# Kernel tuning notes

Hardware: AMD Instinct MI355X
Metric: run time of the kernel (lower is better)

## Reference

```python
import jax, jax.numpy as jnp
import numpy as np

B, N, FEAT, HID, K, GH, GW = 4, 4096, 64, 128, 16, 256, 256


def setup_inputs() -> dict:
    key = jax.random.key(0)
    ks = jax.random.split(key, 16)
    # N distinct grid cells per batch -> unique sparse coordinates (scn active sites)
    cells = jax.vmap(lambda k: jax.random.permutation(k, GH * GW)[:N])(jax.random.split(ks[0], B))
    cy = (cells // GW).astype(jnp.float32)
    cx = (cells % GW).astype(jnp.float32)
    x = cx / GW  # round(x*GW) == cx exactly
    y = cy / GH
    z = jnp.zeros((B, N), jnp.float32)
    p = jax.random.uniform(ks[1], (B, N), jnp.float32)
    xyzp = jnp.stack([x, y, z, p], axis=-1).astype(jnp.float32)
    features = jax.random.normal(ks[2], (B, N, FEAT), jnp.float32)

    def w(k, shape, s=0.05):
        return (jax.random.normal(k, shape) * s).astype(jnp.float32)

    return {
        "xyzp": xyzp, "features": features,
        "ln_g": jnp.ones((FEAT + 2,), jnp.float32), "ln_b": jnp.zeros((FEAT + 2,), jnp.float32),
        "W1": w(ks[3], (9, FEAT + 2, HID)), "b1": jnp.zeros((HID,), jnp.float32),
        "W2": w(ks[4], (9, HID, 3 * HID)),
        "pe_w1": w(ks[5], (3, HID)), "pe_b1": jnp.zeros((HID,), jnp.float32),
        "pe_w2": w(ks[6], (HID, HID)), "pe_b2": jnp.zeros((HID,), jnp.float32),
        "at_w1": w(ks[7], (HID, HID)), "at_b1": jnp.zeros((HID,), jnp.float32),
        "at_w2": w(ks[8], (HID, HID)), "at_b2": jnp.zeros((HID,), jnp.float32),
        "ag_w": w(ks[9], (HID, FEAT)), "ag_b": jnp.zeros((FEAT,), jnp.float32),
        "mlp_w1": w(ks[10], (FEAT, HID)), "mlp_b1": jnp.zeros((HID,), jnp.float32),
        "mlp_w2": w(ks[11], (HID, FEAT)), "mlp_b2": jnp.zeros((FEAT,), jnp.float32),
    }


def _knn_gather(xf, idx):
    # xf: [B,N,C], idx: [B,N,K] -> [B,N,K,C]
    return xf[jnp.arange(xf.shape[0])[:, None, None], idx]


def _forward(xyzp, features, ln_g, ln_b, W1, b1, W2, pe_w1, pe_b1, pe_w2, pe_b2,
             at_w1, at_b1, at_w2, at_b2, ag_w, ag_b, mlp_w1, mlp_b1, mlp_w2, mlp_b2):
    # knn in (x,y,0) space -> 2D squared distances, K nearest (self included, sorted)
    xy = xyzp[..., :2]
    s = jnp.sum(xy * xy, axis=-1)
    d2 = s[:, :, None] + s[:, None, :] - 2.0 * jnp.einsum('bnd,bmd->bnm', xy, xy)
    idx = jax.lax.top_k(-d2, K)[1]  # [B,N,K]

    # positional encoding of (x,y,p) relative offsets
    xyp = jnp.stack([xyzp[..., 0], xyzp[..., 1], xyzp[..., 3]], axis=-1)  # [B,N,3]
    rel = xyp[:, :, None, :] - _knn_gather(xyp, idx)  # [B,N,K,3]
    pe = jax.nn.relu(rel @ pe_w1 + pe_b1) @ pe_w2 + pe_b2  # [B,N,K,HID]

    # polarity split + LayerNorm
    p = (xyzp[..., 3:4] - 0.5) / 0.5
    sp = jnp.concatenate([jnp.clip(p, 0.0, 1.0), -jnp.clip(p, -1.0, 0.0), features], axis=-1)
    mu = jnp.mean(sp, axis=-1, keepdims=True)
    var = jnp.var(sp, axis=-1, keepdims=True)
    sp = (sp - mu) / jnp.sqrt(var + 1e-5) * ln_g + ln_b  # [B,N,FEAT+2]

    # submanifold 3x3 conv x2 via dense index grid (active sites only)
    cy = jnp.round(xyzp[..., 1] * GH).astype(jnp.int32)
    cx = jnp.round(xyzp[..., 0] * GW).astype(jnp.int32)
    bb = jnp.broadcast_to(jnp.arange(B)[:, None], (B, N))
    grid = jnp.full((B, GH + 2, GW + 2), -1, jnp.int32)
    grid = grid.at[bb, cy + 1, cx + 1].set(jnp.broadcast_to(jnp.arange(N, dtype=jnp.int32)[None], (B, N)))
    off = jnp.arange(-1, 2)
    dy = jnp.repeat(off, 3)  # [9]
    dx = jnp.tile(off, 3)    # [9]
    bi = jnp.arange(B)[:, None, None]
    nbr = grid[bi, cy[:, :, None] + 1 + dy, cx[:, :, None] + 1 + dx]  # [B,N,9]
    mask = nbr >= 0
    safe = jnp.where(mask, nbr, 0)
    m = mask[..., None].astype(sp.dtype)

    g1 = sp[bi, safe] * m                                   # [B,N,9,FEAT+2]
    h1 = jnp.einsum('bnkc,kcd->bnd', g1, W1) + b1           # [B,N,HID]
    g2 = h1[bi, safe] * m                                   # [B,N,9,HID]
    h2 = jnp.einsum('bnkc,kcd->bnd', g2, W2)                # [B,N,3*HID]

    qkv = h2.reshape(B, N, HID, 3)  # matches torch reshape([B,N,-1,3])
    q = qkv[..., 0]
    kk = _knn_gather(qkv[..., 1], idx)
    v = _knn_gather(qkv[..., 2], idx)

    # subtraction-based vector attention scored by MLP, softmax over neighbors
    a = q[:, :, None] - kk + pe
    a = jax.nn.relu(a @ at_w1 + at_b1) @ at_w2 + at_b2
    a = jax.nn.softmax(a / jnp.sqrt(jnp.float32(HID)), axis=-2)

    res = jnp.einsum('bmnf,bmnf->bmf', a, v + pe)
    res = res @ ag_w + ag_b + features
    res = jax.nn.gelu(res @ mlp_w1 + mlp_b1, approximate=False) @ mlp_w2 + mlp_b2 + features
    return res


def reference(xyzp, features, ln_g, ln_b, W1, b1, W2, pe_w1, pe_b1, pe_w2, pe_b2,
              at_w1, at_b1, at_w2, at_b2, ag_w, ag_b, mlp_w1, mlp_b1, mlp_w2, mlp_b2):
    return _forward(xyzp, features, ln_g, ln_b, W1, b1, W2, pe_w1, pe_b1, pe_w2, pe_b2,
                    at_w1, at_b1, at_w2, at_b2, ag_w, ag_b, mlp_w1, mlp_b1, mlp_w2, mlp_b2)
```

## Files before the change

### kernel.cpp

```cpp
#include <hip/hip_runtime.h>
#include <math.h>

#define BB 4
#define NN 4096
#define FEAT 64
#define HID 128
#define KNN 16
#define GS 258
#define CIN 66

typedef __attribute__((ext_vector_type(8))) short bf16x8;
typedef __attribute__((ext_vector_type(4))) float f32x4;
#define MFMA_B16(a, b, c) __builtin_amdgcn_mfma_f32_16x16x32_bf16(a, b, c, 0, 0, 0)
#define SWZ(r) ((((r) & 7) << 4) ^ (((r) & 8) << 2))

__device__ __forceinline__ short f2b(float f) {
    unsigned u = __builtin_bit_cast(unsigned, f);
    u = (u + 0x7FFFu + ((u >> 16) & 1u)) >> 16;
    return (short)u;
}
__device__ __forceinline__ float b2f(short s) {
    return __builtin_bit_cast(float, ((unsigned)(unsigned short)s) << 16);
}
__device__ __forceinline__ void gload_lds16(const void* g, void* lds) {
    __builtin_amdgcn_global_load_lds((const __attribute__((address_space(1))) unsigned int*)g,
                                     (__attribute__((address_space(3))) unsigned int*)lds, 16, 0, 0);
}

__global__ __launch_bounds__(256) void k_scatter_sp(const float* __restrict__ xyzp, const float* __restrict__ feat,
                                                    const float* __restrict__ ln_g, const float* __restrict__ ln_b,
                                                    int* __restrict__ grid, int* __restrict__ cxy,
                                                    short* __restrict__ sp_bf) {
    int i = blockIdx.x * 256 + threadIdx.x;
    if (i >= BB * NN) return;
    int b = i / NN;
    float4 xp = *(const float4*)(xyzp + (size_t)i * 4);
    int cx = __float2int_rn(xp.x * 256.0f);
    int cy = __float2int_rn(xp.y * 256.0f);
    cxy[i] = cx | (cy << 8);
    grid[b * GS * GS + (cy + 1) * GS + (cx + 1)] = i % NN;
    float v[CIN];
    float pn = (xp.w - 0.5f) * 2.0f;
    v[0] = fminf(fmaxf(pn, 0.0f), 1.0f);
    v[1] = -fminf(fmaxf(pn, -1.0f), 0.0f);
    const float4* f4 = (const float4*)(feat + (size_t)i * FEAT);
#pragma unroll
    for (int j = 0; j < FEAT / 4; j++) {
        float4 t = f4[j];
        v[2 + 4 * j] = t.x; v[3 + 4 * j] = t.y; v[4 + 4 * j] = t.z; v[5 + 4 * j] = t.w;
    }
    float s = 0.0f;
#pragma unroll
    for (int j = 0; j < CIN; j++) s += v[j];
    float mu = s / (float)CIN;
    float vs = 0.0f;
#pragma unroll
    for (int j = 0; j < CIN; j++) { float d = v[j] - mu; vs += d * d; }
    float inv = 1.0f / sqrtf(vs / (float)CIN + 1e-5f);
    unsigned o2[64];
#pragma unroll
    for (int j = 0; j < 33; j++) {
        float a = (v[2 * j] - mu) * inv * ln_g[2 * j] + ln_b[2 * j];
        float bqq = (2 * j + 1 < CIN) ? ((v[2 * j + 1] - mu) * inv * ln_g[2 * j + 1] + ln_b[2 * j + 1]) : 0.f;
        o2[j] = (unsigned)(unsigned short)f2b(a) | (((unsigned)(unsigned short)f2b(bqq)) << 16);
    }
#pragma unroll
    for (int j = 33; j < 64; j++) o2[j] = 0;
    int4* o = (int4*)(sp_bf + (size_t)i * 128);
#pragma unroll
    for (int t = 0; t < 16; t++) o[t] = make_int4(o2[4 * t], o2[4 * t + 1], o2[4 * t + 2], o2[4 * t + 3]);
}

__device__ __forceinline__ void ins16(unsigned* a, unsigned key) {
    if (key < a[15]) {
#pragma unroll
        for (int j = 15; j >= 1; --j) {
            unsigned prev = a[j - 1];
            a[j] = (prev > key) ? prev : ((a[j] > key) ? key : a[j]);
        }
        a[0] = a[0] < key ? a[0] : key;
    }
}

__device__ __forceinline__ void cmpex(unsigned& x, unsigned& y) {
    unsigned lo = x < y ? x : y;
    unsigned hi = x < y ? y : x;
    x = lo; y = hi;
}

__device__ __forceinline__ void merge16(const unsigned* L, unsigned* c) {
#pragma unroll
    for (int i = 0; i < 16; ++i) c[i] = L[i];
#pragma unroll
    for (int s = 0; s < 4; ++s) {
        int m = 1 << s;
        unsigned bv[16];
#pragma unroll
        for (int i = 0; i < 16; ++i) bv[i] = __shfl_xor(c[15 - i], m);
#pragma unroll
        for (int i = 0; i < 16; ++i) c[i] = c[i] < bv[i] ? c[i] : bv[i];
#pragma unroll
        for (int d = 8; d >= 1; d >>= 1)
#pragma unroll
            for (int i = 0; i < 16; ++i)
                if (!(i & d)) cmpex(c[i], c[i | d]);
    }
}

__global__ __launch_bounds__(256) void k_knn(const int* __restrict__ grid, const int* __restrict__ cxy,
                                             const float* __restrict__ xyzp, float4* __restrict__ relg) {
    int tid = threadIdx.x;
    int t = tid & 15;
    int q = blockIdx.x * 16 + (tid >> 4);
    int b = q >> 12;
    int me = cxy[q];
    int mx = me & 255, my = (me >> 8) & 255;
    const int* gb = grid + b * GS * GS;
    unsigned L[16];
#pragma unroll
    for (int j = 0; j < 16; j++) L[j] = 0xFFFFFFFFu;
    for (int i = t; i < 441; i += 16) {
        int dy = i / 21 - 10, dx = i % 21 - 10;
        int Y = my + dy, X = mx + dx;
        if ((unsigned)Y >= 256u || (unsigned)X >= 256u) continue;
        int j = gb[(Y + 1) * GS + X + 1];
        if (j >= 0) ins16(L, ((unsigned)(dx * dx + dy * dy) << 12) | (unsigned)j);
    }
    unsigned c[16];
    merge16(L, c);
    for (int r = 11; r <= 256; ++r) {
        bool need = (c[15] >> 12) >= (unsigned)(r * r);
        if (!__any(need)) break;
        if (need) {
            int rr = r * r;
            for (int dx = -r + t; dx <= r; dx += 16) {
                int X = mx + dx;
                if ((unsigned)X >= 256u) continue;
                int d2t = dx * dx + rr;
                int Y0 = my - r, Y1 = my + r;
                if ((unsigned)Y0 < 256u) {
                    int j = gb[(Y0 + 1) * GS + X + 1];
                    if (j >= 0) ins16(L, ((unsigned)d2t << 12) | (unsigned)j);
                }
                if ((unsigned)Y1 < 256u) {
                    int j = gb[(Y1 + 1) * GS + X + 1];
                    if (j >= 0) ins16(L, ((unsigned)d2t << 12) | (unsigned)j);
                }
            }
            for (int dy = -r + 1 + t; dy <= r - 1; dy += 16) {
                int Y = my + dy;
                if ((unsigned)Y >= 256u) continue;
                int rowoff = (Y + 1) * GS;
                int d2s = rr + dy * dy;
                int X0 = mx - r, X1 = mx + r;
                if ((unsigned)X0 < 256u) {
                    int j = gb[rowoff + X0 + 1];
                    if (j >= 0) ins16(L, ((unsigned)d2s << 12) | (unsigned)j);
                }
                if ((unsigned)X1 < 256u) {
                    int j = gb[rowoff + X1 + 1];
                    if (j >= 0) ins16(L, ((unsigned)d2s << 12) | (unsigned)j);
                }
            }
            merge16(L, c);
        }
    }
    unsigned mine = 0;
#pragma unroll
    for (int j = 0; j < 16; ++j)
        if (t == j) mine = c[j];
    int g = (b << 12) | (int)(mine & 4095u);
    float4 mef = *(const float4*)(xyzp + (size_t)q * 4);
    float4 tt = *(const float4*)(xyzp + (size_t)g * 4);
    float4 o;
    o.x = mef.x - tt.x; o.y = mef.y - tt.y; o.z = mef.w - tt.w;
    o.w = __int_as_float(g);
    relg[(size_t)q * 16 + t] = o;
}

#define PK128_SZ (4 * 8 * 512)
#define PKW1_SZ (9 * 3 * 8 * 512)
#define PKW2_SZ (9 * 4 * 24 * 512)
#define PACK_TOTAL (3 * PK128_SZ + PKW1_SZ + PKW2_SZ + PK128_SZ + 128)

__global__ __launch_bounds__(256) void k_pack(const float* __restrict__ pe_w2, const float* __restrict__ at_w1,
                                              const float* __restrict__ at_w2, const float* __restrict__ W1,
                                              const float* __restrict__ W2,
                                              const float* __restrict__ pe_b2, const float* __restrict__ at_b1,
                                              short* __restrict__ pk_pe2, short* __restrict__ pk_a1,
                                              short* __restrict__ pk_a2, short* __restrict__ pk_w1,
                                              short* __restrict__ pk_w2, short* __restrict__ pk_wf,
                                              float* __restrict__ cf) {
    int i = blockIdx.x * 256 + threadIdx.x;
    if (i < 3 * PK128_SZ) {
        int seg = i / PK128_SZ, r = i % PK128_SZ;
        int f = r / 512, q = r % 512;
        int lane = q / 8, j = q % 8;
        int kt = f / 8, nt = f % 8;
        int k = kt * 32 + (lane >> 4) * 8 + j, n = nt * 16 + (lane & 15);
        const float* W = (seg == 0) ? pe_w2 : (seg == 1) ? at_w1 : at_w2;
        short* dst = (seg == 0) ? pk_pe2 : (seg == 1) ? pk_a1 : pk_a2;
        dst[r] = f2b(W[k * 128 + n]);
        return;
    }
    i -= 3 * PK128_SZ;
    if (i < PKW1_SZ) {
        int f = i / 512, q = i % 512;
        int lane = q / 8, j = q % 8;
        int tap = f / 24, rem = f % 24;
        int kt = rem / 8, nt = rem % 8;
        int k = kt * 32 + (lane >> 4) * 8 + j, n = nt * 16 + (lane & 15);
        pk_w1[i] = (k < CIN) ? f2b(W1[(tap * CIN + k) * 128 + n]) : (short)0;
        return;
    }
    i -= PKW1_SZ;
    if (i < PKW2_SZ) {
        int f = i / 512, q = i % 512;
        int lane = q / 8, j = q % 8;
        int tap = f / 96, rem = f % 96;
        int kt = rem / 24, nt = rem % 24;
        int k = kt * 32 + (lane >> 4) * 8 + j, n = nt * 16 + (lane & 15);
        pk_w2[i] = f2b(W2[((size_t)(tap * 128 + k)) * 384 + n]);
        return;
    }
    i -= PKW2_SZ;
    if (i < PK128_SZ) {
        int ii = i >> 7, j = i & 127;
        float acc = 0.f;
        for (int m = 0; m < 128; ++m) acc += pe_w2[ii * 128 + m] * at_w1[m * 128 + j];
        int lane = (((ii >> 3) & 3) << 4) | (j & 15);
        int dst = ((ii >> 5) * 8 + (j >> 4)) * 512 + lane * 8 + (ii & 7);
        pk_wf[dst] = f2b(acc);
        return;
    }
    i -= PK128_SZ;
    if (i < 128) {
        float acc = at_b1[i];
        for (int m = 0; m < 128; ++m) acc += pe_b2[m] * at_w1[m * 128 + i];
        cf[i] = acc;
    }
}

__global__ __launch_bounds__(256) void k_conv1(const int* __restrict__ grid, const int* __restrict__ cxy,
                                               const short* __restrict__ sp_bf, const float* __restrict__ b1,
                                               const short* __restrict__ pk_w1, const short* __restrict__ zero256,
                                               short* __restrict__ h1_bf) {
    __shared__ int sj[9][64];
    __shared__ __align__(16) char sb[2][64 * 256];
    int row0 = blockIdx.x * 64;
    int b = row0 / NN;
    int tid = threadIdx.x;
    int w = tid >> 6, l = tid & 63, cl = l & 15;
    for (int e = tid; e < 9 * 64; e += 256) {
        int k = e / 64, p = e % 64;
        int me = cxy[row0 + p];
        sj[k][p] = grid[b * GS * GS + (((me >> 8) & 255) + k / 3) * GS + ((me & 255) + k % 3)];
    }
    __syncthreads();
    f32x4 acc[4][2];
#pragma unroll
    for (int m = 0; m < 4; m++)
#pragma unroll
        for (int nt = 0; nt < 2; nt++) acc[m][nt] = (f32x4){0.f, 0.f, 0.f, 0.f};

#define STAGE1(bufp, tap)                                                                      \
    {                                                                                          \
        _Pragma("unroll") for (int i = 0; i < 4; ++i) {                                        \
            int row = w * 16 + i * 4 + (l >> 4);                                               \
            int j = sj[tap][row];                                                              \
            int srcch = cl ^ (row & 7);                                                        \
            const short* src = (j >= 0) ? (sp_bf + ((size_t)(b * NN + j) * 128 + srcch * 8))   \
                                        : (zero256 + srcch * 8);                               \
            gload_lds16(src, (bufp) + (w * 16 + i * 4) * 256);                                 \
        }                                                                                      \
    }
    STAGE1(&sb[0][0], 0);
    asm volatile("s_waitcnt vmcnt(0)" ::: "memory");
    __syncthreads();
    int cur = 0;
    for (int tap = 0; tap < 9; ++tap) {
        if (tap < 8) STAGE1(&sb[cur ^ 1][0], tap + 1);
        const char* base = &sb[cur][0];
#pragma unroll
        for (int kt = 0; kt < 3; ++kt) {
            bf16x8 a[4];
#pragma unroll
            for (int m = 0; m < 4; ++m) {
                int row = m * 16 + (l & 15);
                a[m] = *(const bf16x8*)&base[row * 256 + ((kt * 64 + (l >> 4) * 16) ^ ((row & 7) << 4))];
            }
#pragma unroll
            for (int nt = 0; nt < 2; ++nt) {
                bf16x8 bv = *(const bf16x8*)(pk_w1 + (size_t)(((tap * 3 + kt) * 8 + w * 2 + nt) * 64 + l) * 8);
#pragma unroll
                for (int m = 0; m < 4; ++m) acc[m][nt] = MFMA_B16(a[m], bv, acc[m][nt]);
            }
        }
        asm volatile("s_waitcnt vmcnt(0)" ::: "memory");
        __syncthreads();
        cur ^= 1;
    }
#pragma unroll
    for (int nt = 0; nt < 2; ++nt) {
        int col = (w * 2 + nt) * 16 + cl;
        float bb = b1[col];
#pragma unroll
        for (int m = 0; m < 4; ++m)
#pragma unroll
            for (int j = 0; j < 4; ++j) {
                int row = row0 + m * 16 + (l >> 4) * 4 + j;
                h1_bf[(size_t)row * 128 + col] = f2b(acc[m][nt][j] + bb);
            }
    }
}

__global__ __launch_bounds__(256) void k_conv2(const int* __restrict__ grid, const int* __restrict__ cxy,
                                               const short* __restrict__ h1_bf, const short* __restrict__ pk_w2,
                                               const short* __restrict__ zero256,
                                               short* __restrict__ qg, short* __restrict__ kg, short* __restrict__ vg) {
    __shared__ int sj[9][64];
    __shared__ __align__(16) char sb[2][64 * 256];
    int bid = blockIdx.x;
    int nb = bid % 3, mb = bid / 3;
    int row0 = mb * 64;
    int b = row0 / NN;
    int tid = threadIdx.x;
    int w = tid >> 6, l = tid & 63, cl = l & 15;
    for (int e = tid; e < 9 * 64; e += 256) {
        int k = e / 64, p = e % 64;
        int me = cxy[row0 + p];
        sj[k][p] = grid[b * GS * GS + (((me >> 8) & 255) + k / 3) * GS + ((me & 255) + k % 3)];
    }
    __syncthreads();
    f32x4 acc[4][2];
#pragma unroll
    for (int m = 0; m < 4; m++)
#pragma unroll
        for (int nt = 0; nt < 2; nt++) acc[m][nt] = (f32x4){0.f, 0.f, 0.f, 0.f};

#define STAGE2(bufp, tap)                                                                      \
    {                                                                                          \
        _Pragma("unroll") for (int i = 0; i < 4; ++i) {                                        \
            int row = w * 16 + i * 4 + (l >> 4);                                               \
            int j = sj[tap][row];                                                              \
            int srcch = cl ^ (row & 7);                                                        \
            const short* src = (j >= 0) ? (h1_bf + ((size_t)(b * NN + j) * 128 + srcch * 8))   \
                                        : (zero256 + srcch * 8);                               \
            gload_lds16(src, (bufp) + (w * 16 + i * 4) * 256);                                 \
        }                                                                                      \
    }
    STAGE2(&sb[0][0], 0);
    asm volatile("s_waitcnt vmcnt(0)" ::: "memory");
    __syncthreads();
    int cur = 0;
    for (int tap = 0; tap < 9; ++tap) {
        if (tap < 8) STAGE2(&sb[cur ^ 1][0], tap + 1);
        const char* base = &sb[cur][0];
#pragma unroll
        for (int kt = 0; kt < 4; ++kt) {
            bf16x8 a[4];
#pragma unroll
            for (int m = 0; m < 4; ++m) {
                int row = m * 16 + (l & 15);
                a[m] = *(const bf16x8*)&base[row * 256 + ((kt * 64 + (l >> 4) * 16) ^ ((row & 7) << 4))];
            }
#pragma unroll
            for (int nt = 0; nt < 2; ++nt) {
                bf16x8 bv = *(const bf16x8*)(pk_w2 + (size_t)(((tap * 4 + kt) * 24 + nb * 8 + w * 2 + nt) * 64 + l) * 8);
#pragma unroll
                for (int m = 0; m < 4; ++m) acc[m][nt] = MFMA_B16(a[m], bv, acc[m][nt]);
            }
        }
        asm volatile("s_waitcnt vmcnt(0)" ::: "memory");
        __syncthreads();
        cur ^= 1;
    }
#pragma unroll
    for (int nt = 0; nt < 2; ++nt) {
        int col = nb * 128 + (w * 2 + nt) * 16 + cl;
        int s = col % 3, dd = col / 3;
        short* dst = (s == 0) ? qg : (s == 1) ? kg : vg;
#pragma unroll
        for (int m = 0; m < 4; ++m)
#pragma unroll
            for (int j = 0; j < 4; ++j) {
                int row = row0 + m * 16 + (l >> 4) * 4 + j;
                dst[(size_t)row * 128 + dd] = f2b(acc[m][nt][j]);
            }
    }
}

__global__ __launch_bounds__(256) void k_qk1(const short* __restrict__ qg, const short* __restrict__ kg,
                                             const short* __restrict__ pk_a1, const float* __restrict__ cf,
                                             short* __restrict__ q1, short* __restrict__ k1) {
    __shared__ __align__(16) char sb[64 * 256];
    int bid = blockIdx.x;
    int qmode = (bid < 256);
    int row0 = (bid & 255) * 64;
    const short* S = qmode ? qg : kg;
    short* O = qmode ? q1 : k1;
    int tid = threadIdx.x;
    int w = tid >> 6, l = tid & 63, cl = l & 15;
    for (int e = tid; e < 1024; e += 256) {
        int row = e >> 4, sl = e & 15;
        gload_lds16(S + ((size_t)(row0 + row) * 128 + (sl ^ (row & 7)) * 8), &sb[e * 16]);
    }
    asm volatile("s_waitcnt vmcnt(0)" ::: "memory");
    __syncthreads();
    f32x4 acc[4][2];
#pragma unroll
    for (int m = 0; m < 4; m++)
#pragma unroll
        for (int nt = 0; nt < 2; nt++) acc[m][nt] = (f32x4){0.f, 0.f, 0.f, 0.f};
#pragma unroll
    for (int kt = 0; kt < 4; ++kt) {
        bf16x8 a[4];
#pragma unroll
        for (int m = 0; m < 4; ++m) {
            int row = m * 16 + (l & 15);
            a[m] = *(const bf16x8*)&sb[row * 256 + ((kt * 64 + (l >> 4) * 16) ^ ((row & 7) << 4))];
        }
#pragma unroll
        for (int nt = 0; nt < 2; ++nt) {
            bf16x8 bv = *(const bf16x8*)(pk_a1 + (size_t)((kt * 8 + w * 2 + nt) * 64 + l) * 8);
#pragma unroll
            for (int m = 0; m < 4; ++m) acc[m][nt] = MFMA_B16(a[m], bv, acc[m][nt]);
        }
    }
#pragma unroll
    for (int nt = 0; nt < 2; ++nt) {
        int col = (w * 2 + nt) * 16 + cl;
        float cv = qmode ? cf[col] : 0.f;
#pragma unroll
        for (int m = 0; m < 4; ++m)
#pragma unroll
            for (int j = 0; j < 4; ++j) {
                int row = row0 + m * 16 + (l >> 4) * 4 + j;
                O[(size_t)row * 128 + col] = f2b(acc[m][nt][j] + cv);
            }
    }
}

__global__ __launch_bounds__(256, 3) void k_attn(const float4* __restrict__ relg,
                                                 const short* __restrict__ q1g, const short* __restrict__ k1g,
                                                 const short* __restrict__ vg,
                                                 const float* __restrict__ pe_w1, const float* __restrict__ pe_b1,
                                                 const float* __restrict__ pe_b2, const float* __restrict__ at_b2,
                                                 const short* __restrict__ pk_pe2, const short* __restrict__ pk_wf,
                                                 const short* __restrict__ pk_a2, float* __restrict__ res1) {
    __shared__ __align__(16) char WK[64 * 256];
    __shared__ float4 s_rel[64];
    __shared__ int s_g[64];
    int tid = threadIdx.x;
    int w = tid >> 6, l = tid & 63, cl = l & 15;
    int P0 = blockIdx.x * 4;

    if (l < 16) {
        float4 f4 = relg[(size_t)(P0 + w) * 16 + l];
        s_rel[w * 16 + l] = f4;
        s_g[w * 16 + l] = __float_as_int(f4.w);
    }
    {
        int c0 = 2 * l;
        float wa0 = pe_w1[c0], wa1 = pe_w1[c0 + 1];
        float wb0 = pe_w1[128 + c0], wb1 = pe_w1[129 + c0];
        float wc0 = pe_w1[256 + c0], wc1 = pe_w1[257 + c0];
        float ba0 = pe_b1[c0], ba1 = pe_b1[c0 + 1];
#pragma unroll
        for (int lr = 0; lr < 16; ++lr) {
            float4 rel = s_rel[w * 16 + lr];
            float h0 = fmaxf(rel.x * wa0 + rel.y * wb0 + rel.z * wc0 + ba0, 0.f);
            float h1v = fmaxf(rel.x * wa1 + rel.y * wb1 + rel.z * wc1 + ba1, 0.f);
            unsigned pk = (unsigned)(unsigned short)f2b(h0) | (((unsigned)(unsigned short)f2b(h1v)) << 16);
            *(unsigned*)&WK[(w * 16 + lr) * 256 + ((4 * l) ^ SWZ(lr))] = pk;
        }
    }
    __syncthreads();
    unsigned k1p[4][4];
    unsigned q1p[4];
#pragma unroll
    for (int m = 0; m < 4; ++m) {
#pragma unroll
        for (int j = 0; j < 4; ++j) {
            int g = s_g[m * 16 + (l >> 4) * 4 + j];
            unsigned lo = *((const unsigned short*)k1g + (size_t)g * 128 + w * 32 + cl);
            unsigned hi = *((const unsigned short*)k1g + (size_t)g * 128 + w * 32 + 16 + cl);
            k1p[m][j] = lo | (hi << 16);
        }
        unsigned qlo = *((const unsigned short*)q1g + (size_t)(P0 + m) * 128 + w * 32 + cl);
        unsigned qhi = *((const unsigned short*)q1g + (size_t)(P0 + m) * 128 + w * 32 + 16 + cl);
        q1p[m] = qlo | (qhi << 16);
    }
    unsigned pe_pk[4][2][2];
    {
        f32x4 pacc[4][2];
#pragma unroll
        for (int m = 0; m < 4; m++)
#pragma unroll
            for (int nt = 0; nt < 2; nt++) pacc[m][nt] = (f32x4){0.f, 0.f, 0.f, 0.f};
#pragma unroll
        for (int kt = 0; kt < 4; ++kt) {
            int off = kt * 64 + (l >> 4) * 16;
            bf16x8 a[4];
#pragma unroll
            for (int m = 0; m < 4; ++m) {
                int ra = m * 16 + (l & 15);
                a[m] = *(const bf16x8*)&WK[ra * 256 + (off ^ SWZ(ra))];
            }
#pragma unroll
            for (int nt = 0; nt < 2; ++nt) {
                bf16x8 bv = *(const bf16x8*)(pk_pe2 + (size_t)((kt * 8 + w * 2 + nt) * 64 + l) * 8);
#pragma unroll
                for (int m = 0; m < 4; ++m) pacc[m][nt] = MFMA_B16(a[m], bv, pacc[m][nt]);
            }
        }
#pragma unroll
        for (int nt = 0; nt < 2; ++nt) {
            float b2v = pe_b2[w * 32 + nt * 16 + cl];
#pragma unroll
            for (int m = 0; m < 4; ++m) {
                float p0v = pacc[m][nt][0] + b2v, p1v = pacc[m][nt][1] + b2v;
                float p2v = pacc[m][nt][2] + b2v, p3v = pacc[m][nt][3] + b2v;
                pe_pk[m][nt][0] = (unsigned)(unsigned short)f2b(p0v) | (((unsigned)(unsigned short)f2b(p1v)) << 16);
                pe_pk[m][nt][1] = (unsigned)(unsigned short)f2b(p2v) | (((unsigned)(unsigned short)f2b(p3v)) << 16);
            }
        }
    }
    f32x4 facc[4][2];
#pragma unroll
    for (int m = 0; m < 4; m++)
#pragma unroll
        for (int nt = 0; nt < 2; nt++) facc[m][nt] = (f32x4){0.f, 0.f, 0.f, 0.f};
#pragma unroll
    for (int kt = 0; kt < 4; ++kt) {
        int off = kt * 64 + (l >> 4) * 16;
        bf16x8 a[4];
#pragma unroll
        for (int m = 0; m < 4; ++m) {
            int ra = m * 16 + (l & 15);
            a[m] = *(const bf16x8*)&WK[ra * 256 + (off ^ SWZ(ra))];
        }
#pragma unroll
        for (int nt = 0; nt < 2; ++nt) {
            bf16x8 bv = *(const bf16x8*)(pk_wf + (size_t)((kt * 8 + w * 2 + nt) * 64 + l) * 8);
#pragma unroll
            for (int m = 0; m < 4; ++m) facc[m][nt] = MFMA_B16(a[m], bv, facc[m][nt]);
        }
    }
    __syncthreads();
#pragma unroll
    for (int m = 0; m < 4; ++m)
#pragma unroll
        for (int nt = 0; nt < 2; ++nt) {
            int col = w * 32 + nt * 16 + cl;
            float qv = b2f((short)((q1p[m] >> (nt * 16)) & 0xffff));
#pragma unroll
            for (int j = 0; j < 4; ++j) {
                int rr = m * 16 + (l >> 4) * 4 + j;
                float kv = b2f((short)((k1p[m][j] >> (nt * 16)) & 0xffff));
                float x = facc[m][nt][j] + qv - kv;
                *(short*)&WK[rr * 256 + ((col * 2) ^ SWZ(rr))] = f2b(fmaxf(x, 0.f));
            }
        }
    unsigned vp[4][4];
#pragma unroll
    for (int m = 0; m < 4; ++m)
#pragma unroll
        for (int j = 0; j < 4; ++j) {
            int g = s_g[m * 16 + (l >> 4) * 4 + j];
            unsigned lo = *((const unsigned short*)vg + (size_t)g * 128 + w * 32 + cl);
            unsigned hi = *((const unsigned short*)vg + (size_t)g * 128 + w * 32 + 16 + cl);
            vp[m][j] = lo | (hi << 16);
        }
    __syncthreads();
#pragma unroll
    for (int m = 0; m < 4; m++)
#pragma unroll
        for (int nt = 0; nt < 2; nt++) facc[m][nt] = (f32x4){0.f, 0.f, 0.f, 0.f};
#pragma unroll
    for (int kt = 0; kt < 4; ++kt) {
        int off = kt * 64 + (l >> 4) * 16;
        bf16x8 a[4];
#pragma unroll
        for (int m = 0; m < 4; ++m) {
            int ra = m * 16 + (l & 15);
            a[m] = *(const bf16x8*)&WK[ra * 256 + (off ^ SWZ(ra))];
        }
#pragma unroll
        for (int nt = 0; nt < 2; ++nt) {
            bf16x8 bv = *(const bf16x8*)(pk_a2 + (size_t)((kt * 8 + w * 2 + nt) * 64 + l) * 8);
#pragma unroll
            for (int m = 0; m < 4; ++m) facc[m][nt] = MFMA_B16(a[m], bv, facc[m][nt]);
        }
    }
    const float scale = 0.08838834764831845f;
#pragma unroll
    for (int m = 0; m < 4; ++m)
#pragma unroll
        for (int nt = 0; nt < 2; ++nt) {
            int col = w * 32 + nt * 16 + cl;
            float bv = at_b2[col];
            float sv[4];
#pragma unroll
            for (int j = 0; j < 4; ++j) sv[j] = (facc[m][nt][j] + bv) * scale;
            float mx = fmaxf(fmaxf(sv[0], sv[1]), fmaxf(sv[2], sv[3]));
            mx = fmaxf(mx, __shfl_xor(mx, 16));
            mx = fmaxf(mx, __shfl_xor(mx, 32));
            float ee[4], es = 0.f;
#pragma unroll
            for (int j = 0; j < 4; ++j) { ee[j] = __expf(sv[j] - mx); es += ee[j]; }
            es += __shfl_xor(es, 16);
            es += __shfl_xor(es, 32);
            float pev[4];
            pev[0] = b2f((short)(pe_pk[m][nt][0] & 0xffff));
            pev[1] = b2f((short)(pe_pk[m][nt][0] >> 16));
            pev[2] = b2f((short)(pe_pk[m][nt][1] & 0xffff));
            pev[3] = b2f((short)(pe_pk[m][nt][1] >> 16));
            float o = 0.f;
#pragma unroll
            for (int j = 0; j < 4; ++j) {
                float vvv = b2f((short)((vp[m][j] >> (nt * 16)) & 0xffff));
                o += ee[j] * (vvv + pev[j]);
            }
            o += __shfl_xor(o, 16);
            o += __shfl_xor(o, 32);
            if (l < 16) res1[(size_t)(P0 + m) * 128 + col] = o / es;
        }
}

__global__ __launch_bounds__(256) void k_head(const float* __restrict__ res1, const float* __restrict__ feat,
                                              const float* __restrict__ ag_w, const float* __restrict__ ag_b,
                                              const float* __restrict__ mlp_w1, const float* __restrict__ mlp_b1,
                                              const float* __restrict__ mlp_w2, const float* __restrict__ mlp_b2,
                                              float* __restrict__ out) {
    __shared__ __align__(16) float rs[64][128];
    __shared__ __align__(16) float r1s[64][64];
    int tid = threadIdx.x;
    int i0 = blockIdx.x * 64;
    for (int e = tid; e < 64 * 128; e += 256) rs[e >> 7][e & 127] = res1[(size_t)i0 * 128 + e];
    __syncthreads();
    {
        int d = tid & 63, rg = tid >> 6;
        float acc[16];
#pragma unroll
        for (int i = 0; i < 16; i++) acc[i] = 0.0f;
        for (int c4 = 0; c4 < 32; ++c4) {
            int c = c4 * 4;
            float w0 = ag_w[c * 64 + d], w1 = ag_w[(c + 1) * 64 + d];
            float w2 = ag_w[(c + 2) * 64 + d], w3 = ag_w[(c + 3) * 64 + d];
#pragma unroll
            for (int i = 0; i < 16; i++) {
                float4 f = *(const float4*)&rs[rg * 16 + i][c];
                acc[i] += f.x * w0 + f.y * w1 + f.z * w2 + f.w * w3;
            }
        }
        float bb = ag_b[d];
#pragma unroll
        for (int i = 0; i < 16; i++) {
            int pp = rg * 16 + i;
            r1s[pp][d] = acc[i] + bb + feat[(size_t)(i0 + pp) * 64 + d];
        }
    }
    __syncthreads();
    {
        int d = tid & 127, rg = tid >> 7;
        float acc[32];
#pragma unroll
        for (int i = 0; i < 32; i++) acc[i] = 0.0f;
        for (int c4 = 0; c4 < 16; ++c4) {
            int c = c4 * 4;
            float w0 = mlp_w1[c * 128 + d], w1 = mlp_w1[(c + 1) * 128 + d];
            float w2 = mlp_w1[(c + 2) * 128 + d], w3 = mlp_w1[(c + 3) * 128 + d];
#pragma unroll
            for (int i = 0; i < 32; i++) {
                float4 f = *(const float4*)&r1s[rg * 32 + i][c];
                acc[i] += f.x * w0 + f.y * w1 + f.z * w2 + f.w * w3;
            }
        }
        float bb = mlp_b1[d];
#pragma unroll
        for (int i = 0; i < 32; i++) {
            float x = acc[i] + bb;
            rs[rg * 32 + i][d] = 0.5f * x * (1.0f + erff(x * 0.70710678118654752f));
        }
    }
    __syncthreads();
    {
        int d = tid & 63, rg = tid >> 6;
        float acc[16];
#pragma unroll
        for (int i = 0; i < 16; i++) acc[i] = 0.0f;
        for (int c4 = 0; c4 < 32; ++c4) {
            int c = c4 * 4;
            float w0 = mlp_w2[c * 64 + d], w1 = mlp_w2[(c + 1) * 64 + d];
            float w2 = mlp_w2[(c + 2) * 64 + d], w3 = mlp_w2[(c + 3) * 64 + d];
#pragma unroll
            for (int i = 0; i < 16; i++) {
                float4 f = *(const float4*)&rs[rg * 16 + i][c];
                acc[i] += f.x * w0 + f.y * w1 + f.z * w2 + f.w * w3;
            }
        }
        float bb = mlp_b2[d];
#pragma unroll
        for (int i = 0; i < 16; i++) {
            int pp = rg * 16 + i;
            out[(size_t)(i0 + pp) * 64 + d] = acc[i] + bb + feat[(size_t)(i0 + pp) * 64 + d];
        }
    }
}

extern "C" void kernel_launch(void* const* d_in, const int* in_sizes, int n_in,
                              void* d_out, int out_size, void* d_ws, size_t ws_size,
                              hipStream_t stream) {
    const float* xyzp = (const float*)d_in[0];
    const float* features = (const float*)d_in[1];
    const float* ln_g = (const float*)d_in[2];
    const float* ln_b = (const float*)d_in[3];
    const float* W1 = (const float*)d_in[4];
    const float* b1 = (const float*)d_in[5];
    const float* W2 = (const float*)d_in[6];
    const float* pe_w1 = (const float*)d_in[7];
    const float* pe_b1 = (const float*)d_in[8];
    const float* pe_w2 = (const float*)d_in[9];
    const float* pe_b2 = (const float*)d_in[10];
    const float* at_w1 = (const float*)d_in[11];
    const float* at_b1 = (const float*)d_in[12];
    const float* at_w2 = (const float*)d_in[13];
    const float* at_b2 = (const float*)d_in[14];
    const float* ag_w = (const float*)d_in[15];
    const float* ag_b = (const float*)d_in[16];
    const float* mlp_w1 = (const float*)d_in[17];
    const float* mlp_b1 = (const float*)d_in[18];
    const float* mlp_w2 = (const float*)d_in[19];
    const float* mlp_b2 = (const float*)d_in[20];
    float* out = (float*)d_out;

    char* w = (char*)d_ws;
    auto alloc = [&](size_t bytes) { char* pp = w; w += (bytes + 255) & ~(size_t)255; return pp; };
    int* grid = (int*)alloc((size_t)BB * GS * GS * 4);
    short* zero256 = (short*)alloc(256);
    int* cxy = (int*)alloc((size_t)BB * NN * 4);
    float4* relg = (float4*)alloc((size_t)BB * NN * KNN * 16);
    short* sp_bf = (short*)alloc((size_t)BB * NN * 128 * 2);
    short* h1_bf = (short*)alloc((size_t)BB * NN * HID * 2);
    short* qg = (short*)alloc((size_t)BB * NN * HID * 2);
    short* kg = (short*)alloc((size_t)BB * NN * HID * 2);
    short* vg = (short*)alloc((size_t)BB * NN * HID * 2);
    short* q1 = (short*)alloc((size_t)BB * NN * HID * 2);
    short* k1 = (short*)alloc((size_t)BB * NN * HID * 2);
    float* res1 = (float*)alloc((size_t)BB * NN * HID * 4);
    short* pk_pe2 = (short*)alloc((size_t)PK128_SZ * 2);
    short* pk_a1 = (short*)alloc((size_t)PK128_SZ * 2);
    short* pk_a2 = (short*)alloc((size_t)PK128_SZ * 2);
    short* pk_wf = (short*)alloc((size_t)PK128_SZ * 2);
    short* pk_w1 = (short*)alloc((size_t)PKW1_SZ * 2);
    short* pk_w2 = (short*)alloc((size_t)PKW2_SZ * 2);
    float* cf = (float*)alloc(128 * 4);

    hipMemsetAsync(grid, 0xFF, (size_t)BB * GS * GS * 4, stream);
    hipMemsetAsync(zero256, 0, 256, stream);
    k_scatter_sp<<<(BB * NN + 255) / 256, 256, 0, stream>>>(xyzp, features, ln_g, ln_b, grid, cxy, sp_bf);
    k_pack<<<(PACK_TOTAL + 255) / 256, 256, 0, stream>>>(
        pe_w2, at_w1, at_w2, W1, W2, pe_b2, at_b1, pk_pe2, pk_a1, pk_a2, pk_w1, pk_w2, pk_wf, cf);
    k_knn<<<BB * NN / 16, 256, 0, stream>>>(grid, cxy, xyzp, relg);
    k_conv1<<<BB * NN / 64, 256, 0, stream>>>(grid, cxy, sp_bf, b1, pk_w1, zero256, h1_bf);
    k_conv2<<<(BB * NN / 64) * 3, 256, 0, stream>>>(grid, cxy, h1_bf, pk_w2, zero256, qg, kg, vg);
    k_qk1<<<512, 256, 0, stream>>>(qg, kg, pk_a1, cf, q1, k1);
    k_attn<<<BB * NN / 4, 256, 0, stream>>>(relg, q1, k1, vg, pe_w1, pe_b1, pe_b2, at_b2,
                                            pk_pe2, pk_wf, pk_a2, res1);
    k_head<<<BB * NN / 64, 256, 0, stream>>>(res1, features, ag_w, ag_b, mlp_w1, mlp_b1, mlp_w2, mlp_b2, out);
}
```

Measured before the change: 211.2 us.

## Fold at_w1 into conv2 weights, drop qk1 kernel, MFMA head

Premultiplies the q and k column blocks of W2 by at_w1 at pack time, so conv2 writes q1/k1 directly and the separate k_qk1 GEMM kernel and its intermediate buffers are removed. The head kernel's three scalar fp32 GEMMs are rewritten as bf16 MFMA with prepacked weights, and the attention output is stored as bf16 to halve its traffic. The trade-off is extra per-call pack work: a 128-term dot product per element of the packed W2. It also adds bf16 rounding in the head path.

```diff
diff --git a/kernel.cpp b/kernel.cpp
--- a/kernel.cpp
+++ b/kernel.cpp
@@ -181,16 +181,20 @@
 #define PK128_SZ (4 * 8 * 512)
 #define PKW1_SZ (9 * 3 * 8 * 512)
 #define PKW2_SZ (9 * 4 * 24 * 512)
-#define PACK_TOTAL (3 * PK128_SZ + PKW1_SZ + PKW2_SZ + PK128_SZ + 128)
+#define PKH_SZ 8192
+#define PACK_TOTAL (3 * PK128_SZ + PKW1_SZ + PKW2_SZ + PK128_SZ + 128 + 3 * PKH_SZ)
 
 __global__ __launch_bounds__(256) void k_pack(const float* __restrict__ pe_w2, const float* __restrict__ at_w1,
                                               const float* __restrict__ at_w2, const float* __restrict__ W1,
                                               const float* __restrict__ W2,
                                               const float* __restrict__ pe_b2, const float* __restrict__ at_b1,
+                                              const float* __restrict__ ag_w, const float* __restrict__ mlp_w1,
+                                              const float* __restrict__ mlp_w2,
                                               short* __restrict__ pk_pe2, short* __restrict__ pk_a1,
                                               short* __restrict__ pk_a2, short* __restrict__ pk_w1,
                                               short* __restrict__ pk_w2, short* __restrict__ pk_wf,
-                                              float* __restrict__ cf) {
+                                              float* __restrict__ cf, short* __restrict__ pk_ag,
+                                              short* __restrict__ pk_m1, short* __restrict__ pk_m2) {
     int i = blockIdx.x * 256 + threadIdx.x;
     if (i < 3 * PK128_SZ) {
         int seg = i / PK128_SZ, r = i % PK128_SZ;
@@ -220,7 +224,16 @@
         int tap = f / 96, rem = f % 96;
         int kt = rem / 24, nt = rem % 24;
         int k = kt * 32 + (lane >> 4) * 8 + j, n = nt * 16 + (lane & 15);
-        pk_w2[i] = f2b(W2[((size_t)(tap * 128 + k)) * 384 + n]);
+        float acc;
+        if (n < 256) {
+            int sel = n >> 7, cc = n & 127;
+            acc = 0.f;
+            for (int m = 0; m < 128; ++m)
+                acc += W2[((size_t)(tap * 128 + k)) * 384 + 3 * m + sel] * at_w1[m * 128 + cc];
+        } else {
+            acc = W2[((size_t)(tap * 128 + k)) * 384 + 3 * (n - 256) + 2];
+        }
+        pk_w2[i] = f2b(acc);
         return;
     }
     i -= PKW2_SZ;
@@ -238,6 +251,33 @@
         float acc = at_b1[i];
         for (int m = 0; m < 128; ++m) acc += pe_b2[m] * at_w1[m * 128 + i];
         cf[i] = acc;
+        return;
+    }
+    i -= 128;
+    if (i < PKH_SZ) {
+        int f = i / 512, q = i % 512;
+        int lane = q / 8, j = q % 8;
+        int kt = f >> 2, nt = f & 3;
+        int k = kt * 32 + (lane >> 4) * 8 + j, n = nt * 16 + (lane & 15);
+        pk_ag[i] = f2b(ag_w[k * 64 + n]);
+        return;
+    }
+    i -= PKH_SZ;
+    if (i < PKH_SZ) {
+        int f = i / 512, q = i % 512;
+        int lane = q / 8, j = q % 8;
+        int kt = f >> 3, nt = f & 7;
+        int k = kt * 32 + (lane >> 4) * 8 + j, n = nt * 16 + (lane & 15);
+        pk_m1[i] = f2b(mlp_w1[k * 128 + n]);
+        return;
+    }
+    i -= PKH_SZ;
+    if (i < PKH_SZ) {
+        int f = i / 512, q = i % 512;
+        int lane = q / 8, j = q % 8;
+        int kt = f >> 2, nt = f & 3;
+        int k = kt * 32 + (lane >> 4) * 8 + j, n = nt * 16 + (lane & 15);
+        pk_m2[i] = f2b(mlp_w2[k * 64 + n]);
     }
 }
 
@@ -316,8 +356,8 @@
 
 __global__ __launch_bounds__(256) void k_conv2(const int* __restrict__ grid, const int* __restrict__ cxy,
                                                const short* __restrict__ h1_bf, const short* __restrict__ pk_w2,
-                                               const short* __restrict__ zero256,
-                                               short* __restrict__ qg, short* __restrict__ kg, short* __restrict__ vg) {
+                                               const short* __restrict__ zero256, const float* __restrict__ cf,
+                                               short* __restrict__ q1, short* __restrict__ k1, short* __restrict__ vg) {
     __shared__ int sj[9][64];
     __shared__ __align__(16) char sb[2][64 * 256];
     int bid = blockIdx.x;
@@ -378,65 +418,15 @@
 #pragma unroll
     for (int nt = 0; nt < 2; ++nt) {
         int col = nb * 128 + (w * 2 + nt) * 16 + cl;
-        int s = col % 3, dd = col / 3;
-        short* dst = (s == 0) ? qg : (s == 1) ? kg : vg;
+        int seg = col >> 7, dd = col & 127;
+        short* dst = (seg == 0) ? q1 : (seg == 1) ? k1 : vg;
+        float cadd = (seg == 0) ? cf[dd] : 0.f;
 #pragma unroll
         for (int m = 0; m < 4; ++m)
 #pragma unroll
             for (int j = 0; j < 4; ++j) {
                 int row = row0 + m * 16 + (l >> 4) * 4 + j;
-                dst[(size_t)row * 128 + dd] = f2b(acc[m][nt][j]);
-            }
-    }
-}
-
-__global__ __launch_bounds__(256) void k_qk1(const short* __restrict__ qg, const short* __restrict__ kg,
-                                             const short* __restrict__ pk_a1, const float* __restrict__ cf,
-                                             short* __restrict__ q1, short* __restrict__ k1) {
-    __shared__ __align__(16) char sb[64 * 256];
-    int bid = blockIdx.x;
-    int qmode = (bid < 256);
-    int row0 = (bid & 255) * 64;
-    const short* S = qmode ? qg : kg;
-    short* O = qmode ? q1 : k1;
-    int tid = threadIdx.x;
-    int w = tid >> 6, l = tid & 63, cl = l & 15;
-    for (int e = tid; e < 1024; e += 256) {
-        int row = e >> 4, sl = e & 15;
-        gload_lds16(S + ((size_t)(row0 + row) * 128 + (sl ^ (row & 7)) * 8), &sb[e * 16]);
-    }
-    asm volatile("s_waitcnt vmcnt(0)" ::: "memory");
-    __syncthreads();
-    f32x4 acc[4][2];
-#pragma unroll
-    for (int m = 0; m < 4; m++)
-#pragma unroll
-        for (int nt = 0; nt < 2; nt++) acc[m][nt] = (f32x4){0.f, 0.f, 0.f, 0.f};
-#pragma unroll
-    for (int kt = 0; kt < 4; ++kt) {
-        bf16x8 a[4];
-#pragma unroll
-        for (int m = 0; m < 4; ++m) {
-            int row = m * 16 + (l & 15);
-            a[m] = *(const bf16x8*)&sb[row * 256 + ((kt * 64 + (l >> 4) * 16) ^ ((row & 7) << 4))];
-        }
-#pragma unroll
-        for (int nt = 0; nt < 2; ++nt) {
-            bf16x8 bv = *(const bf16x8*)(pk_a1 + (size_t)((kt * 8 + w * 2 + nt) * 64 + l) * 8);
-#pragma unroll
-            for (int m = 0; m < 4; ++m) acc[m][nt] = MFMA_B16(a[m], bv, acc[m][nt]);
-        }
-    }
-#pragma unroll
-    for (int nt = 0; nt < 2; ++nt) {
-        int col = (w * 2 + nt) * 16 + cl;
-        float cv = qmode ? cf[col] : 0.f;
-#pragma unroll
-        for (int m = 0; m < 4; ++m)
-#pragma unroll
-            for (int j = 0; j < 4; ++j) {
-                int row = row0 + m * 16 + (l >> 4) * 4 + j;
-                O[(size_t)row * 128 + col] = f2b(acc[m][nt][j] + cv);
+                dst[(size_t)row * 128 + dd] = f2b(acc[m][nt][j] + cadd);
             }
     }
 }
@@ -447,7 +437,7 @@
                                                  const float* __restrict__ pe_w1, const float* __restrict__ pe_b1,
                                                  const float* __restrict__ pe_b2, const float* __restrict__ at_b2,
                                                  const short* __restrict__ pk_pe2, const short* __restrict__ pk_wf,
-                                                 const short* __restrict__ pk_a2, float* __restrict__ res1) {
+                                                 const short* __restrict__ pk_a2, short* __restrict__ res1b) {
     __shared__ __align__(16) char WK[64 * 256];
     __shared__ float4 s_rel[64];
     __shared__ int s_g[64];
@@ -624,88 +614,116 @@
             }
             o += __shfl_xor(o, 16);
             o += __shfl_xor(o, 32);
-            if (l < 16) res1[(size_t)(P0 + m) * 128 + col] = o / es;
-        }
-}
-
-__global__ __launch_bounds__(256) void k_head(const float* __restrict__ res1, const float* __restrict__ feat,
-                                              const float* __restrict__ ag_w, const float* __restrict__ ag_b,
-                                              const float* __restrict__ mlp_w1, const float* __restrict__ mlp_b1,
-                                              const float* __restrict__ mlp_w2, const float* __restrict__ mlp_b2,
-                                              float* __restrict__ out) {
-    __shared__ __align__(16) float rs[64][128];
-    __shared__ __align__(16) float r1s[64][64];
+            if (l < 16) res1b[(size_t)(P0 + m) * 128 + col] = f2b(o / es);
+        }
+}
+
+__global__ __launch_bounds__(256) void k_head(const short* __restrict__ res1b, const float* __restrict__ feat,
+                                              const float* __restrict__ ag_b, const float* __restrict__ mlp_b1,
+                                              const float* __restrict__ mlp_b2,
+                                              const short* __restrict__ pk_ag, const short* __restrict__ pk_m1,
+                                              const short* __restrict__ pk_m2, float* __restrict__ out) {
+    __shared__ __align__(16) char sA[64 * 256];
+    __shared__ __align__(16) char r1s[64 * 128];
     int tid = threadIdx.x;
+    int w = tid >> 6, l = tid & 63, cl = l & 15;
     int i0 = blockIdx.x * 64;
-    for (int e = tid; e < 64 * 128; e += 256) rs[e >> 7][e & 127] = res1[(size_t)i0 * 128 + e];
+    for (int e = tid; e < 1024; e += 256) {
+        int row = e >> 4, sl = e & 15;
+        gload_lds16(res1b + ((size_t)(i0 + row) * 128 + (sl ^ (row & 7)) * 8), &sA[e * 16]);
+    }
+    asm volatile("s_waitcnt vmcnt(0)" ::: "memory");
     __syncthreads();
     {
-        int d = tid & 63, rg = tid >> 6;
-        float acc[16];
-#pragma unroll
-        for (int i = 0; i < 16; i++) acc[i] = 0.0f;
-        for (int c4 = 0; c4 < 32; ++c4) {
-            int c = c4 * 4;
-            float w0 = ag_w[c * 64 + d], w1 = ag_w[(c + 1) * 64 + d];
-            float w2 = ag_w[(c + 2) * 64 + d], w3 = ag_w[(c + 3) * 64 + d];
-#pragma unroll
-            for (int i = 0; i < 16; i++) {
-                float4 f = *(const float4*)&rs[rg * 16 + i][c];
-                acc[i] += f.x * w0 + f.y * w1 + f.z * w2 + f.w * w3;
-            }
-        }
-        float bb = ag_b[d];
-#pragma unroll
-        for (int i = 0; i < 16; i++) {
-            int pp = rg * 16 + i;
-            r1s[pp][d] = acc[i] + bb + feat[(size_t)(i0 + pp) * 64 + d];
-        }
+        f32x4 acc[4];
+#pragma unroll
+        for (int m = 0; m < 4; m++) acc[m] = (f32x4){0.f, 0.f, 0.f, 0.f};
+#pragma unroll
+        for (int kt = 0; kt < 4; ++kt) {
+            bf16x8 a[4];
+#pragma unroll
+            for (int m = 0; m < 4; ++m) {
+                int row = m * 16 + (l & 15);
+                a[m] = *(const bf16x8*)&sA[row * 256 + ((kt * 64 + (l >> 4) * 16) ^ ((row & 7) << 4))];
+            }
+            bf16x8 bv = *(const bf16x8*)(pk_ag + (size_t)((kt * 4 + w) * 64 + l) * 8);
+#pragma unroll
+            for (int m = 0; m < 4; ++m) acc[m] = MFMA_B16(a[m], bv, acc[m]);
+        }
+        int col = w * 16 + cl;
+        float bb = ag_b[col];
+#pragma unroll
+        for (int m = 0; m < 4; ++m)
+#pragma unroll
+            for (int j = 0; j < 4; ++j) {
+                int row = m * 16 + (l >> 4) * 4 + j;
+                float val = acc[m][j] + bb + feat[(size_t)(i0 + row) * 64 + col];
+                *(short*)&r1s[row * 128 + ((col * 2) ^ ((row & 7) << 4))] = f2b(val);
+            }
     }
     __syncthreads();
     {
-        int d = tid & 127, rg = tid >> 7;
-        float acc[32];
-#pragma unroll
-        for (int i = 0; i < 32; i++) acc[i] = 0.0f;
-        for (int c4 = 0; c4 < 16; ++c4) {
-            int c = c4 * 4;
-            float w0 = mlp_w1[c * 128 + d], w1 = mlp_w1[(c + 1) * 128 + d];
-            float w2 = mlp_w1[(c + 2) * 128 + d], w3 = mlp_w1[(c + 3) * 128 + d];
-#pragma unroll
-            for (int i = 0; i < 32; i++) {
-                float4 f = *(const float4*)&r1s[rg * 32 + i][c];
-                acc[i] += f.x * w0 + f.y * w1 + f.z * w2 + f.w * w3;
-            }
-        }
-        float bb = mlp_b1[d];
-#pragma unroll
-        for (int i = 0; i < 32; i++) {
-            float x = acc[i] + bb;
-            rs[rg * 32 + i][d] = 0.5f * x * (1.0f + erff(x * 0.70710678118654752f));
+        f32x4 acc[4][2];
+#pragma unroll
+        for (int m = 0; m < 4; m++)
+#pragma unroll
+            for (int nt = 0; nt < 2; nt++) acc[m][nt] = (f32x4){0.f, 0.f, 0.f, 0.f};
+#pragma unroll
+        for (int kt = 0; kt < 2; ++kt) {
+            bf16x8 a[4];
+#pragma unroll
+            for (int m = 0; m < 4; ++m) {
+                int row = m * 16 + (l & 15);
+                a[m] = *(const bf16x8*)&r1s[row * 128 + ((kt * 64 + (l >> 4) * 16) ^ ((row & 7) << 4))];
+            }
+#pragma unroll
+            for (int nt = 0; nt < 2; ++nt) {
+                bf16x8 bv = *(const bf16x8*)(pk_m1 + (size_t)((kt * 8 + w * 2 + nt) * 64 + l) * 8);
+#pragma unroll
+                for (int m = 0; m < 4; ++m) acc[m][nt] = MFMA_B16(a[m], bv, acc[m][nt]);
+            }
+        }
+#pragma unroll
+        for (int nt = 0; nt < 2; ++nt) {
+            int col = (w * 2 + nt) * 16 + cl;
+            float bb = mlp_b1[col];
+#pragma unroll
+            for (int m = 0; m < 4; ++m)
+#pragma unroll
+                for (int j = 0; j < 4; ++j) {
+                    int row = m * 16 + (l >> 4) * 4 + j;
+                    float x = acc[m][nt][j] + bb;
+                    float g = 0.5f * x * (1.0f + erff(x * 0.70710678118654752f));
+                    *(short*)&sA[row * 256 + ((col * 2) ^ ((row & 7) << 4))] = f2b(g);
+                }
         }
     }
     __syncthreads();
     {
-        int d = tid & 63, rg = tid >> 6;
-        float acc[16];
-#pragma unroll
-        for (int i = 0; i < 16; i++) acc[i] = 0.0f;
-        for (int c4 = 0; c4 < 32; ++c4) {
-            int c = c4 * 4;
-            float w0 = mlp_w2[c * 64 + d], w1 = mlp_w2[(c + 1) * 64 + d];
-            float w2 = mlp_w2[(c + 2) * 64 + d], w3 = mlp_w2[(c + 3) * 64 + d];
-#pragma unroll
-            for (int i = 0; i < 16; i++) {
-                float4 f = *(const float4*)&rs[rg * 16 + i][c];
-                acc[i] += f.x * w0 + f.y * w1 + f.z * w2 + f.w * w3;
-            }
-        }
-        float bb = mlp_b2[d];
-#pragma unroll
-        for (int i = 0; i < 16; i++) {
-            int pp = rg * 16 + i;
-            out[(size_t)(i0 + pp) * 64 + d] = acc[i] + bb + feat[(size_t)(i0 + pp) * 64 + d];
-        }
+        f32x4 acc[4];
+#pragma unroll
+        for (int m = 0; m < 4; m++) acc[m] = (f32x4){0.f, 0.f, 0.f, 0.f};
+#pragma unroll
+        for (int kt = 0; kt < 4; ++kt) {
+            bf16x8 a[4];
+#pragma unroll
+            for (int m = 0; m < 4; ++m) {
+                int row = m * 16 + (l & 15);
+                a[m] = *(const bf16x8*)&sA[row * 256 + ((kt * 64 + (l >> 4) * 16) ^ ((row & 7) << 4))];
+            }
+            bf16x8 bv = *(const bf16x8*)(pk_m2 + (size_t)((kt * 4 + w) * 64 + l) * 8);
+#pragma unroll
+            for (int m = 0; m < 4; ++m) acc[m] = MFMA_B16(a[m], bv, acc[m]);
+        }
+        int col = w * 16 + cl;
+        float bb = mlp_b2[col];
+#pragma unroll
+        for (int m = 0; m < 4; ++m)
+#pragma unroll
+            for (int j = 0; j < 4; ++j) {
+                int row = m * 16 + (l >> 4) * 4 + j;
+                out[(size_t)(i0 + row) * 64 + col] = acc[m][j] + bb + feat[(size_t)(i0 + row) * 64 + col];
+            }
     }
 }
 
@@ -743,30 +761,31 @@
     float4* relg = (float4*)alloc((size_t)BB * NN * KNN * 16);
     short* sp_bf = (short*)alloc((size_t)BB * NN * 128 * 2);
     short* h1_bf = (short*)alloc((size_t)BB * NN * HID * 2);
-    short* qg = (short*)alloc((size_t)BB * NN * HID * 2);
-    short* kg = (short*)alloc((size_t)BB * NN * HID * 2);
-    short* vg = (short*)alloc((size_t)BB * NN * HID * 2);
     short* q1 = (short*)alloc((size_t)BB * NN * HID * 2);
     short* k1 = (short*)alloc((size_t)BB * NN * HID * 2);
-    float* res1 = (float*)alloc((size_t)BB * NN * HID * 4);
+    short* vg = (short*)alloc((size_t)BB * NN * HID * 2);
+    short* res1b = (short*)alloc((size_t)BB * NN * HID * 2);
     short* pk_pe2 = (short*)alloc((size_t)PK128_SZ * 2);
     short* pk_a1 = (short*)alloc((size_t)PK128_SZ * 2);
     short* pk_a2 = (short*)alloc((size_t)PK128_SZ * 2);
     short* pk_wf = (short*)alloc((size_t)PK128_SZ * 2);
     short* pk_w1 = (short*)alloc((size_t)PKW1_SZ * 2);
     short* pk_w2 = (short*)alloc((size_t)PKW2_SZ * 2);
+    short* pk_ag = (short*)alloc((size_t)PKH_SZ * 2);
+    short* pk_m1 = (short*)alloc((size_t)PKH_SZ * 2);
+    short* pk_m2 = (short*)alloc((size_t)PKH_SZ * 2);
     float* cf = (float*)alloc(128 * 4);
 
     hipMemsetAsync(grid, 0xFF, (size_t)BB * GS * GS * 4, stream);
     hipMemsetAsync(zero256, 0, 256, stream);
     k_scatter_sp<<<(BB * NN + 255) / 256, 256, 0, stream>>>(xyzp, features, ln_g, ln_b, grid, cxy, sp_bf);
     k_pack<<<(PACK_TOTAL + 255) / 256, 256, 0, stream>>>(
-        pe_w2, at_w1, at_w2, W1, W2, pe_b2, at_b1, pk_pe2, pk_a1, pk_a2, pk_w1, pk_w2, pk_wf, cf);
+        pe_w2, at_w1, at_w2, W1, W2, pe_b2, at_b1, ag_w, mlp_w1, mlp_w2,
+        pk_pe2, pk_a1, pk_a2, pk_w1, pk_w2, pk_wf, cf, pk_ag, pk_m1, pk_m2);
     k_knn<<<BB * NN / 16, 256, 0, stream>>>(grid, cxy, xyzp, relg);
     k_conv1<<<BB * NN / 64, 256, 0, stream>>>(grid, cxy, sp_bf, b1, pk_w1, zero256, h1_bf);
-    k_conv2<<<(BB * NN / 64) * 3, 256, 0, stream>>>(grid, cxy, h1_bf, pk_w2, zero256, qg, kg, vg);
-    k_qk1<<<512, 256, 0, stream>>>(qg, kg, pk_a1, cf, q1, k1);
+    k_conv2<<<(BB * NN / 64) * 3, 256, 0, stream>>>(grid, cxy, h1_bf, pk_w2, zero256, cf, q1, k1, vg);
     k_attn<<<BB * NN / 4, 256, 0, stream>>>(relg, q1, k1, vg, pe_w1, pe_b1, pe_b2, at_b2,
-                                            pk_pe2, pk_wf, pk_a2, res1);
-    k_head<<<BB * NN / 64, 256, 0, stream>>>(res1, features, ag_w, ag_b, mlp_w1, mlp_b1, mlp_w2, mlp_b2, out);
-}
+                                            pk_pe2, pk_wf, pk_a2, res1b);
+    k_head<<<BB * NN / 64, 256, 0, stream>>>(res1b, features, ag_b, mlp_b1, mlp_b2, pk_ag, pk_m1, pk_m2, out);
+}
```

Result: faster. 207.1 us (-2.0%).
